# Kernel tuning notes

Hardware: AMD Instinct MI355X
Metric: run time of the kernel (lower is better)

Reference implementation:

```python
import jax, jax.numpy as jnp
import numpy as np

MARGIN = 0.25
SCALE = 64.0
OP = 1.0 + MARGIN
ON = -MARGIN
DELTA_P = 1.0 - MARGIN
DELTA_N = MARGIN
NEG_FILL = -1e4  # effectively -inf for these logits (|logit| < ~300)

B, D = 8192, 1024
N_IDS = 512


def setup_inputs() -> dict:
    key = jax.random.key(0)
    k1, k2 = jax.random.split(key)
    inputs = jax.random.normal(k1, (B, D), dtype=jnp.float32)
    targets = jax.random.randint(k2, (B,), 0, N_IDS, dtype=jnp.int64)
    return {"inputs": inputs, "targets": targets}


def reference(inputs, targets):
    # L2-normalize embeddings (torch F.normalize uses eps=1e-12 clamp on norm)
    norm = jnp.maximum(jnp.linalg.norm(inputs, axis=1, keepdims=True), 1e-12)
    x = inputs / norm
    sim = x @ x.T  # [B, B] cosine similarities

    same = targets[:, None] == targets[None, :]
    eye = jnp.eye(targets.shape[0], dtype=bool)
    pos_mask = same & ~eye
    neg_mask = ~same

    sim_sg = jax.lax.stop_gradient(sim)  # .detach() in original
    ap = jnp.maximum(OP - sim_sg, 0.0)
    an = jnp.maximum(sim_sg - ON, 0.0)

    logit_p = -ap * (sim - DELTA_P) * SCALE
    logit_n = an * (sim - DELTA_N) * SCALE

    lse_p = jax.nn.logsumexp(jnp.where(pos_mask, logit_p, NEG_FILL), axis=1)
    lse_n = jax.nn.logsumexp(jnp.where(neg_mask, logit_n, NEG_FILL), axis=1)

    loss_i = jax.nn.softplus(lse_n + lse_p)  # [B]
    valid = pos_mask.any(axis=1) & neg_mask.any(axis=1)

    total = jnp.sum(jnp.where(valid, loss_i, 0.0))
    count = jnp.maximum(jnp.sum(valid), 1)
    return total / count
```

## Files before the change

### kernel.cpp

```cpp
#include <hip/hip_runtime.h>
#include <hip/hip_bf16.h>
#include <math.h>

#define THREADS 256
typedef unsigned short ushortT;
typedef __attribute__((ext_vector_type(8))) short bf16x8;
typedef __attribute__((ext_vector_type(4))) float f32x4;

__device__ __forceinline__ void async16(const ushortT* g, ushortT* l) {
  __builtin_amdgcn_global_load_lds(
      (const __attribute__((address_space(1))) unsigned int*)g,
      (__attribute__((address_space(3))) unsigned int*)l, 16, 0, 0);
}

__device__ __forceinline__ ushortT f2bf(float f) {
  __hip_bfloat16 h = __float2bfloat16(f);
  return *reinterpret_cast<ushortT*>(&h);
}

__global__ __launch_bounds__(THREADS) void k_prep(const float* __restrict__ x,
                                                  ushortT* __restrict__ xn, int D) {
  __shared__ float red[4];
  const int row = blockIdx.x;
  const int tid = threadIdx.x;
  const int gid = row * (D / 4) + tid;
  const float4 v = reinterpret_cast<const float4*>(x)[gid];
  float s = v.x * v.x + v.y * v.y + v.z * v.z + v.w * v.w;
  #pragma unroll
  for (int off = 32; off; off >>= 1) s += __shfl_xor(s, off);
  if ((tid & 63) == 0) red[tid >> 6] = s;
  __syncthreads();
  const float tot = red[0] + red[1] + red[2] + red[3];
  const float rn = 1.0f / fmaxf(sqrtf(tot), 1e-12f);
  ushort4 o;
  o.x = f2bf(v.x * rn); o.y = f2bf(v.y * rn);
  o.z = f2bf(v.z * rn); o.w = f2bf(v.w * rn);
  reinterpret_cast<ushort4*>(xn)[gid] = o;
}

__global__ __launch_bounds__(THREADS, 2) void k_main_mfma(const ushortT* __restrict__ xn,
                                                          const int* __restrict__ tgt,
                                                          float4* __restrict__ partial,
                                                          int D, int nb) {
  __shared__ ushortT Asm[2][128 * 32];
  __shared__ ushortT Bsm[2][128 * 32];

  const int tid = threadIdx.x;
  const int lane = tid & 63;
  const int w = tid >> 6;

  const int b = blockIdx.x;
  int bi = (int)((2.f * nb + 1.f -
                  sqrtf((2.f * nb + 1.f) * (2.f * nb + 1.f) - 8.f * (float)b)) * 0.5f);
  while ((bi + 1) * (2 * nb - bi) / 2 <= b) ++bi;
  while (bi * (2 * nb - bi + 1) / 2 > b) --bi;
  const int bj = bi + (b - bi * (2 * nb - bi + 1) / 2);
  const bool isdiag = (bi == bj);

  const int i0 = bi * 128, j0 = bj * 128;
  const int wr = (w >> 1) * 64, wc = (w & 1) * 64;

  const int sr = lane & 15, sc = lane >> 4;
  const ushortT* baseA = xn + (size_t)i0 * D;
  const ushortT* baseB = xn + (size_t)j0 * D;
  const int offA = (w * 16 + sr) * D + sc * 8;
  const int hstep = 64 * D;

  const int aoff = ((w >> 1) * 4) * 512 + lane * 8;
  const int boff = ((w & 1) * 4) * 512 + lane * 8;

  f32x4 acc[4][4];
  #pragma unroll
  for (int mt = 0; mt < 4; ++mt)
    #pragma unroll
    for (int nt = 0; nt < 4; ++nt)
      acc[mt][nt] = (f32x4){0.f, 0.f, 0.f, 0.f};

  const int kiters = D / 32;

  {
    async16(baseA + offA, &Asm[0][w * 512]);
    async16(baseA + offA + hstep, &Asm[0][(w + 4) * 512]);
    if (!isdiag) {
      async16(baseB + offA, &Bsm[0][w * 512]);
      async16(baseB + offA + hstep, &Bsm[0][(w + 4) * 512]);
    }
  }
  __syncthreads();

  int cur = 0;
  for (int kk = 0; kk < kiters; ++kk) {
    if (kk + 1 < kiters) {
      const int ko = (kk + 1) * 32;
      const int nxt = cur ^ 1;
      async16(baseA + offA + ko, &Asm[nxt][w * 512]);
      async16(baseA + offA + hstep + ko, &Asm[nxt][(w + 4) * 512]);
      if (!isdiag) {
        async16(baseB + offA + ko, &Bsm[nxt][w * 512]);
        async16(baseB + offA + hstep + ko, &Bsm[nxt][(w + 4) * 512]);
      }
    }

    const ushortT* Ab = Asm[cur];
    const ushortT* Bb = isdiag ? Asm[cur] : Bsm[cur];
    bf16x8 afr[4];
    #pragma unroll
    for (int mt = 0; mt < 4; ++mt)
      afr[mt] = *reinterpret_cast<const bf16x8*>(&Ab[aoff + mt * 512]);
    {
      bf16x8 b0 = *reinterpret_cast<const bf16x8*>(&Bb[boff]);
      bf16x8 b1 = *reinterpret_cast<const bf16x8*>(&Bb[boff + 512]);
      #pragma unroll
      for (int mt = 0; mt < 4; ++mt)
        acc[mt][0] = __builtin_amdgcn_mfma_f32_16x16x32_bf16(afr[mt], b0, acc[mt][0], 0, 0, 0);
      #pragma unroll
      for (int mt = 0; mt < 4; ++mt)
        acc[mt][1] = __builtin_amdgcn_mfma_f32_16x16x32_bf16(afr[mt], b1, acc[mt][1], 0, 0, 0);
      b0 = *reinterpret_cast<const bf16x8*>(&Bb[boff + 2 * 512]);
      b1 = *reinterpret_cast<const bf16x8*>(&Bb[boff + 3 * 512]);
      #pragma unroll
      for (int mt = 0; mt < 4; ++mt)
        acc[mt][2] = __builtin_amdgcn_mfma_f32_16x16x32_bf16(afr[mt], b0, acc[mt][2], 0, 0, 0);
      #pragma unroll
      for (int mt = 0; mt < 4; ++mt)
        acc[mt][3] = __builtin_amdgcn_mfma_f32_16x16x32_bf16(afr[mt], b1, acc[mt][3], 0, 0, 0);
    }
    __syncthreads();
    cur ^= 1;
  }

  const int q = lane >> 4, c = lane & 15;
  int tj[4];
  #pragma unroll
  for (int nt = 0; nt < 4; ++nt) tj[nt] = tgt[j0 + wc + nt * 16 + c];
  int tir[16];
  #pragma unroll
  for (int mt = 0; mt < 4; ++mt) {
    const int4 t4 = *reinterpret_cast<const int4*>(tgt + i0 + wr + mt * 16 + q * 4);
    tir[mt * 4 + 0] = t4.x; tir[mt * 4 + 1] = t4.y;
    tir[mt * 4 + 2] = t4.z; tir[mt * 4 + 3] = t4.w;
  }

  #pragma unroll
  for (int mt = 0; mt < 4; ++mt) {
    #pragma unroll
    for (int reg = 0; reg < 4; ++reg) {
      const int i = i0 + wr + mt * 16 + q * 4 + reg;
      const int ti = tir[mt * 4 + reg];
      float m = -1e30f, sn = 0.f;
      float sel[4];
      #pragma unroll
      for (int nt = 0; nt < 4; ++nt) {
        const float s = acc[mt][nt][reg];
        const int j = j0 + wc + nt * 16 + c;
        const bool same = (tj[nt] == ti);
        const bool vpos = same && (j != i);
        const float lp = (fminf(s, 1.25f) - 1.25f) * fmaf(s, 64.f, -48.f);
        const float sv = vpos ? lp : -2e30f;
        sel[nt] = sv;
        m = fmaxf(m, sv);
        const float ln = (fmaxf(s, -0.25f) + 0.25f) * fmaf(s, 64.f, -16.f);
        const float en = __expf(ln);
        sn += same ? 0.f : en;
      }
      #pragma unroll
      for (int off = 1; off < 16; off <<= 1) m = fmaxf(m, __shfl_xor(m, off));
      float sp = 0.f;
      #pragma unroll
      for (int nt = 0; nt < 4; ++nt) sp += __expf(sel[nt] - m);
      #pragma unroll
      for (int off = 1; off < 16; off <<= 1) {
        sp += __shfl_xor(sp, off);
        sn += __shfl_xor(sn, off);
      }
      if (c == 0) {
        float4 o; o.x = m; o.y = sp; o.z = 0.f; o.w = sn;
        partial[((size_t)i * nb + bj) * 2 + (w & 1)] = o;
      }
    }
  }

  if (!isdiag) {
    #pragma unroll
    for (int nt = 0; nt < 4; ++nt) {
      const int jt = tj[nt];
      const int jrow = j0 + wc + nt * 16 + c;
      float m = -1e30f, sn = 0.f;
      #pragma unroll
      for (int mt = 0; mt < 4; ++mt) {
        #pragma unroll
        for (int reg = 0; reg < 4; ++reg) {
          const float s = acc[mt][nt][reg];
          const bool same = (tir[mt * 4 + reg] == jt);
          const float lp = (fminf(s, 1.25f) - 1.25f) * fmaf(s, 64.f, -48.f);
          m = fmaxf(m, same ? lp : -2e30f);
          const float ln = (fmaxf(s, -0.25f) + 0.25f) * fmaf(s, 64.f, -16.f);
          const float en = __expf(ln);
          sn += same ? 0.f : en;
        }
      }
      m = fmaxf(m, __shfl_xor(m, 16));
      m = fmaxf(m, __shfl_xor(m, 32));
      float sp = 0.f;
      #pragma unroll
      for (int mt = 0; mt < 4; ++mt) {
        #pragma unroll
        for (int reg = 0; reg < 4; ++reg) {
          const float s = acc[mt][nt][reg];
          const bool same = (tir[mt * 4 + reg] == jt);
          const float lp = (fminf(s, 1.25f) - 1.25f) * fmaf(s, 64.f, -48.f);
          sp += __expf((same ? lp : -2e30f) - m);
        }
      }
      sp += __shfl_xor(sp, 16); sp += __shfl_xor(sp, 32);
      sn += __shfl_xor(sn, 16); sn += __shfl_xor(sn, 32);
      if (lane < 16) {
        float4 o; o.x = m; o.y = sp; o.z = 0.f; o.w = sn;
        partial[((size_t)jrow * nb + bi) * 2 + (w >> 1)] = o;
      }
    }
  }
}

__global__ __launch_bounds__(THREADS) void k_reduce(const float4* __restrict__ partial,
                                                    float* __restrict__ row_loss) {
  const int lane = threadIdx.x & 63;
  const int row = blockIdx.x * 4 + (threadIdx.x >> 6);
  const float4 a = partial[(size_t)row * 128 + lane];
  const float4 b = partial[(size_t)row * 128 + 64 + lane];
  float mp = fmaxf(a.x, b.x);
  float sp = a.y * __expf(a.x - mp) + b.y * __expf(b.x - mp);
  float sn = a.w + b.w;
  #pragma unroll
  for (int off = 1; off < 64; off <<= 1) {
    const float m2 = __shfl_xor(mp, off), s2 = __shfl_xor(sp, off);
    const float nm = fmaxf(mp, m2);
    sp = sp * __expf(mp - nm) + s2 * __expf(m2 - nm);
    mp = nm;
    sn += __shfl_xor(sn, off);
  }
  if (lane == 0) {
    float loss = -1.0f;
    if (sp > 0.f && sn > 0.f) {
      const float z = mp + logf(sp) + logf(sn);
      loss = (z > 0.f) ? (z + log1pf(__expf(-z))) : log1pf(__expf(z));
    }
    row_loss[row] = loss;
  }
}

__global__ __launch_bounds__(THREADS) void k_final(const float* __restrict__ row_loss,
                                                   float* __restrict__ out, int B) {
  __shared__ float ssum[4];
  __shared__ float scnt[4];
  const int tid = threadIdx.x;
  float sum = 0.f, cnt = 0.f;
  for (int i = tid; i < B; i += THREADS) {
    const float l = row_loss[i];
    if (l >= 0.f) { sum += l; cnt += 1.f; }
  }
  #pragma unroll
  for (int off = 32; off; off >>= 1) {
    sum += __shfl_xor(sum, off);
    cnt += __shfl_xor(cnt, off);
  }
  if ((tid & 63) == 0) { ssum[tid >> 6] = sum; scnt[tid >> 6] = cnt; }
  __syncthreads();
  if (tid == 0) {
    float ts = 0.f, tc = 0.f;
    #pragma unroll
    for (int w = 0; w < 4; ++w) { ts += ssum[w]; tc += scnt[w]; }
    out[0] = ts / fmaxf(tc, 1.f);
  }
}

extern "C" void kernel_launch(void* const* d_in, const int* in_sizes, int n_in,
                              void* d_out, int out_size, void* d_ws, size_t ws_size,
                              hipStream_t stream) {
  const float* x = (const float*)d_in[0];
  const int* tgt = (const int*)d_in[1];
  float* out = (float*)d_out;
  const int B = in_sizes[1];
  const int D = in_sizes[0] / B;
  const int nb = B / 128;

  ushortT* xn = (ushortT*)d_ws;
  float4* partial = (float4*)((char*)d_ws + (size_t)B * D * 2);
  float* row_loss = (float*)((char*)d_ws + (size_t)B * D * 2 + (size_t)B * 2 * nb * 16);

  k_prep<<<B, THREADS, 0, stream>>>(x, xn, D);
  k_main_mfma<<<nb * (nb + 1) / 2, THREADS, 0, stream>>>(xn, tgt, partial, D, nb);
  k_reduce<<<B / 4, THREADS, 0, stream>>>(partial, row_loss);
  k_final<<<1, THREADS, 0, stream>>>(row_loss, out, B);
}
```

Measured before the change: 251.8 us.

## Enlarge GEMM tile to 256x256 with 8 waves and K-step 64

The main kernel moves from 128x128 tiles with 4 waves to 256x256 tiles with 8 waves (512 threads). Each wave now computes a 128x64 sub-tile, and each stage loads 64 K values with double-buffered LDS. The aim is more data reuse per LDS/global load and fewer tile blocks and syncs. The partial layout is remapped onto 128-column chunks, with a dummy entry written for the transposed path so k_reduce can stay unchanged. In exchange, the 128 accumulator floats per thread plus fragments raise register pressure, and far fewer blocks (528) may leave CUs underused.

```diff
diff --git a/kernel.cpp b/kernel.cpp
--- a/kernel.cpp
+++ b/kernel.cpp
@@ -3,6 +3,7 @@
 #include <math.h>
 
 #define THREADS 256
+#define MTHREADS 512
 typedef unsigned short ushortT;
 typedef __attribute__((ext_vector_type(8))) short bf16x8;
 typedef __attribute__((ext_vector_type(4))) float f32x4;
@@ -38,12 +39,12 @@
   reinterpret_cast<ushort4*>(xn)[gid] = o;
 }
 
-__global__ __launch_bounds__(THREADS, 2) void k_main_mfma(const ushortT* __restrict__ xn,
-                                                          const int* __restrict__ tgt,
-                                                          float4* __restrict__ partial,
-                                                          int D, int nb) {
-  __shared__ ushortT Asm[2][128 * 32];
-  __shared__ ushortT Bsm[2][128 * 32];
+__global__ __launch_bounds__(MTHREADS, 2) void k_main_mfma(const ushortT* __restrict__ xn,
+                                                           const int* __restrict__ tgt,
+                                                           float4* __restrict__ partial,
+                                                           int D, int nb) {
+  __shared__ ushortT Asm[2][16 * 1024];
+  __shared__ ushortT Bsm[2][16 * 1024];
 
   const int tid = threadIdx.x;
   const int lane = tid & 63;
@@ -57,73 +58,75 @@
   const int bj = bi + (b - bi * (2 * nb - bi + 1) / 2);
   const bool isdiag = (bi == bj);
 
-  const int i0 = bi * 128, j0 = bj * 128;
-  const int wr = (w >> 1) * 64, wc = (w & 1) * 64;
+  const int i0 = bi * 256, j0 = bj * 256;
+  const int wr2 = w >> 2;
+  const int wc2 = w & 3;
+  const int ib = i0 + wr2 * 128;
+  const int jb = j0 + wc2 * 64;
+  const int nbp = nb * 2;
 
   const int sr = lane & 15, sc = lane >> 4;
-  const ushortT* baseA = xn + (size_t)i0 * D;
-  const ushortT* baseB = xn + (size_t)j0 * D;
-  const int offA = (w * 16 + sr) * D + sc * 8;
-  const int hstep = 64 * D;
-
-  const int aoff = ((w >> 1) * 4) * 512 + lane * 8;
-  const int boff = ((w & 1) * 4) * 512 + lane * 8;
-
-  f32x4 acc[4][4];
-  #pragma unroll
-  for (int mt = 0; mt < 4; ++mt)
+  const ushortT* gA0 = xn + (size_t)(i0 + w * 16 + sr) * D + sc * 8;
+  const ushortT* gA1 = gA0 + (size_t)128 * D;
+  const ushortT* gB0 = xn + (size_t)(j0 + w * 16 + sr) * D + sc * 8;
+  const ushortT* gB1 = gB0 + (size_t)128 * D;
+
+  f32x4 acc[8][4];
+  #pragma unroll
+  for (int mt = 0; mt < 8; ++mt)
     #pragma unroll
     for (int nt = 0; nt < 4; ++nt)
       acc[mt][nt] = (f32x4){0.f, 0.f, 0.f, 0.f};
 
-  const int kiters = D / 32;
+  const int kiters = D / 64;
+  int cur = 0;
 
   {
-    async16(baseA + offA, &Asm[0][w * 512]);
-    async16(baseA + offA + hstep, &Asm[0][(w + 4) * 512]);
+    async16(gA0, &Asm[0][w * 1024]);
+    async16(gA0 + 32, &Asm[0][w * 1024 + 512]);
+    async16(gA1, &Asm[0][(w + 8) * 1024]);
+    async16(gA1 + 32, &Asm[0][(w + 8) * 1024 + 512]);
     if (!isdiag) {
-      async16(baseB + offA, &Bsm[0][w * 512]);
-      async16(baseB + offA + hstep, &Bsm[0][(w + 4) * 512]);
+      async16(gB0, &Bsm[0][w * 1024]);
+      async16(gB0 + 32, &Bsm[0][w * 1024 + 512]);
+      async16(gB1, &Bsm[0][(w + 8) * 1024]);
+      async16(gB1 + 32, &Bsm[0][(w + 8) * 1024 + 512]);
     }
   }
   __syncthreads();
 
-  int cur = 0;
   for (int kk = 0; kk < kiters; ++kk) {
     if (kk + 1 < kiters) {
-      const int ko = (kk + 1) * 32;
+      const size_t ko = (size_t)(kk + 1) * 64;
       const int nxt = cur ^ 1;
-      async16(baseA + offA + ko, &Asm[nxt][w * 512]);
-      async16(baseA + offA + hstep + ko, &Asm[nxt][(w + 4) * 512]);
+      async16(gA0 + ko, &Asm[nxt][w * 1024]);
+      async16(gA0 + ko + 32, &Asm[nxt][w * 1024 + 512]);
+      async16(gA1 + ko, &Asm[nxt][(w + 8) * 1024]);
+      async16(gA1 + ko + 32, &Asm[nxt][(w + 8) * 1024 + 512]);
       if (!isdiag) {
-        async16(baseB + offA + ko, &Bsm[nxt][w * 512]);
-        async16(baseB + offA + hstep + ko, &Bsm[nxt][(w + 4) * 512]);
-      }
-    }
-
+        async16(gB0 + ko, &Bsm[nxt][w * 1024]);
+        async16(gB0 + ko + 32, &Bsm[nxt][w * 1024 + 512]);
+        async16(gB1 + ko, &Bsm[nxt][(w + 8) * 1024]);
+        async16(gB1 + ko + 32, &Bsm[nxt][(w + 8) * 1024 + 512]);
+      }
+    }
     const ushortT* Ab = Asm[cur];
     const ushortT* Bb = isdiag ? Asm[cur] : Bsm[cur];
-    bf16x8 afr[4];
-    #pragma unroll
-    for (int mt = 0; mt < 4; ++mt)
-      afr[mt] = *reinterpret_cast<const bf16x8*>(&Ab[aoff + mt * 512]);
-    {
-      bf16x8 b0 = *reinterpret_cast<const bf16x8*>(&Bb[boff]);
-      bf16x8 b1 = *reinterpret_cast<const bf16x8*>(&Bb[boff + 512]);
-      #pragma unroll
-      for (int mt = 0; mt < 4; ++mt)
-        acc[mt][0] = __builtin_amdgcn_mfma_f32_16x16x32_bf16(afr[mt], b0, acc[mt][0], 0, 0, 0);
-      #pragma unroll
-      for (int mt = 0; mt < 4; ++mt)
-        acc[mt][1] = __builtin_amdgcn_mfma_f32_16x16x32_bf16(afr[mt], b1, acc[mt][1], 0, 0, 0);
-      b0 = *reinterpret_cast<const bf16x8*>(&Bb[boff + 2 * 512]);
-      b1 = *reinterpret_cast<const bf16x8*>(&Bb[boff + 3 * 512]);
-      #pragma unroll
-      for (int mt = 0; mt < 4; ++mt)
-        acc[mt][2] = __builtin_amdgcn_mfma_f32_16x16x32_bf16(afr[mt], b0, acc[mt][2], 0, 0, 0);
-      #pragma unroll
-      for (int mt = 0; mt < 4; ++mt)
-        acc[mt][3] = __builtin_amdgcn_mfma_f32_16x16x32_bf16(afr[mt], b1, acc[mt][3], 0, 0, 0);
+    #pragma unroll
+    for (int s = 0; s < 2; ++s) {
+      bf16x8 afr[8];
+      #pragma unroll
+      for (int mt = 0; mt < 8; ++mt)
+        afr[mt] = *reinterpret_cast<const bf16x8*>(&Ab[(wr2 * 8 + mt) * 1024 + s * 512 + lane * 8]);
+      bf16x8 bfr[4];
+      #pragma unroll
+      for (int nt = 0; nt < 4; ++nt)
+        bfr[nt] = *reinterpret_cast<const bf16x8*>(&Bb[(wc2 * 4 + nt) * 1024 + s * 512 + lane * 8]);
+      #pragma unroll
+      for (int mt = 0; mt < 8; ++mt)
+        #pragma unroll
+        for (int nt = 0; nt < 4; ++nt)
+          acc[mt][nt] = __builtin_amdgcn_mfma_f32_16x16x32_bf16(afr[mt], bfr[nt], acc[mt][nt], 0, 0, 0);
     }
     __syncthreads();
     cur ^= 1;
@@ -132,27 +135,24 @@
   const int q = lane >> 4, c = lane & 15;
   int tj[4];
   #pragma unroll
-  for (int nt = 0; nt < 4; ++nt) tj[nt] = tgt[j0 + wc + nt * 16 + c];
-  int tir[16];
-  #pragma unroll
-  for (int mt = 0; mt < 4; ++mt) {
-    const int4 t4 = *reinterpret_cast<const int4*>(tgt + i0 + wr + mt * 16 + q * 4);
-    tir[mt * 4 + 0] = t4.x; tir[mt * 4 + 1] = t4.y;
-    tir[mt * 4 + 2] = t4.z; tir[mt * 4 + 3] = t4.w;
-  }
-
-  #pragma unroll
-  for (int mt = 0; mt < 4; ++mt) {
+  for (int nt = 0; nt < 4; ++nt) tj[nt] = tgt[jb + nt * 16 + c];
+
+  const int cb1 = bj * 2 + (wc2 >> 1);
+  const int half1 = wc2 & 1;
+  #pragma unroll
+  for (int mt = 0; mt < 8; ++mt) {
+    const int4 t4 = *reinterpret_cast<const int4*>(tgt + ib + mt * 16 + q * 4);
+    const int tiq[4] = {t4.x, t4.y, t4.z, t4.w};
     #pragma unroll
     for (int reg = 0; reg < 4; ++reg) {
-      const int i = i0 + wr + mt * 16 + q * 4 + reg;
-      const int ti = tir[mt * 4 + reg];
+      const int i = ib + mt * 16 + q * 4 + reg;
+      const int ti = tiq[reg];
       float m = -1e30f, sn = 0.f;
       float sel[4];
       #pragma unroll
       for (int nt = 0; nt < 4; ++nt) {
         const float s = acc[mt][nt][reg];
-        const int j = j0 + wc + nt * 16 + c;
+        const int j = jb + nt * 16 + c;
         const bool same = (tj[nt] == ti);
         const bool vpos = same && (j != i);
         const float lp = (fminf(s, 1.25f) - 1.25f) * fmaf(s, 64.f, -48.f);
@@ -175,23 +175,26 @@
       }
       if (c == 0) {
         float4 o; o.x = m; o.y = sp; o.z = 0.f; o.w = sn;
-        partial[((size_t)i * nb + bj) * 2 + (w & 1)] = o;
+        partial[((size_t)i * nbp + cb1) * 2 + half1] = o;
       }
     }
   }
 
   if (!isdiag) {
+    const int cb2 = bi * 2 + wr2;
     #pragma unroll
     for (int nt = 0; nt < 4; ++nt) {
       const int jt = tj[nt];
-      const int jrow = j0 + wc + nt * 16 + c;
+      const int jrow = jb + nt * 16 + c;
       float m = -1e30f, sn = 0.f;
       #pragma unroll
-      for (int mt = 0; mt < 4; ++mt) {
+      for (int mt = 0; mt < 8; ++mt) {
+        const int4 t4 = *reinterpret_cast<const int4*>(tgt + ib + mt * 16 + q * 4);
+        const int tiq[4] = {t4.x, t4.y, t4.z, t4.w};
         #pragma unroll
         for (int reg = 0; reg < 4; ++reg) {
           const float s = acc[mt][nt][reg];
-          const bool same = (tir[mt * 4 + reg] == jt);
+          const bool same = (tiq[reg] == jt);
           const float lp = (fminf(s, 1.25f) - 1.25f) * fmaf(s, 64.f, -48.f);
           m = fmaxf(m, same ? lp : -2e30f);
           const float ln = (fmaxf(s, -0.25f) + 0.25f) * fmaf(s, 64.f, -16.f);
@@ -203,11 +206,13 @@
       m = fmaxf(m, __shfl_xor(m, 32));
       float sp = 0.f;
       #pragma unroll
-      for (int mt = 0; mt < 4; ++mt) {
+      for (int mt = 0; mt < 8; ++mt) {
+        const int4 t4 = *reinterpret_cast<const int4*>(tgt + ib + mt * 16 + q * 4);
+        const int tiq[4] = {t4.x, t4.y, t4.z, t4.w};
         #pragma unroll
         for (int reg = 0; reg < 4; ++reg) {
           const float s = acc[mt][nt][reg];
-          const bool same = (tir[mt * 4 + reg] == jt);
+          const bool same = (tiq[reg] == jt);
           const float lp = (fminf(s, 1.25f) - 1.25f) * fmaf(s, 64.f, -48.f);
           sp += __expf((same ? lp : -2e30f) - m);
         }
@@ -216,7 +221,9 @@
       sn += __shfl_xor(sn, 16); sn += __shfl_xor(sn, 32);
       if (lane < 16) {
         float4 o; o.x = m; o.y = sp; o.z = 0.f; o.w = sn;
-        partial[((size_t)jrow * nb + bi) * 2 + (w >> 1)] = o;
+        partial[((size_t)jrow * nbp + cb2) * 2 + 0] = o;
+        float4 z; z.x = -1e30f; z.y = 0.f; z.z = 0.f; z.w = 0.f;
+        partial[((size_t)jrow * nbp + cb2) * 2 + 1] = z;
       }
     }
   }
@@ -282,14 +289,15 @@
   float* out = (float*)d_out;
   const int B = in_sizes[1];
   const int D = in_sizes[0] / B;
-  const int nb = B / 128;
+  const int nb128 = B / 128;
+  const int nb256 = B / 256;
 
   ushortT* xn = (ushortT*)d_ws;
   float4* partial = (float4*)((char*)d_ws + (size_t)B * D * 2);
-  float* row_loss = (float*)((char*)d_ws + (size_t)B * D * 2 + (size_t)B * 2 * nb * 16);
+  float* row_loss = (float*)((char*)d_ws + (size_t)B * D * 2 + (size_t)B * 2 * nb128 * 16);
 
   k_prep<<<B, THREADS, 0, stream>>>(x, xn, D);
-  k_main_mfma<<<nb * (nb + 1) / 2, THREADS, 0, stream>>>(xn, tgt, partial, D, nb);
+  k_main_mfma<<<nb256 * (nb256 + 1) / 2, MTHREADS, 0, stream>>>(xn, tgt, partial, D, nb256);
   k_reduce<<<B / 4, THREADS, 0, stream>>>(partial, row_loss);
   k_final<<<1, THREADS, 0, stream>>>(row_loss, out, B);
 }
```

Result: slower. 296.8 us (+17.9%).
